# Kernel optimization log

Hardware: AMD Instinct MI355X
Metric: run time of the kernel (lower is better)

The kernel has to match this reference:

```python
import jax, jax.numpy as jnp
import numpy as np

MU = 0.99
THRESHOLD = 1.0


def setup_inputs() -> dict:
    key = jax.random.key(0)
    k1, k2, k3 = jax.random.split(key, 3)
    N, D, T, K = 8, 64, 8192, 2048
    x = jax.random.normal(k1, (N, D, T), dtype=jnp.float32)
    k = jax.random.normal(k2, (K, D), dtype=jnp.float32)
    k_sum = jax.random.normal(k3, (K, D), dtype=jnp.float32)
    k_elem = jnp.ones((K,), dtype=jnp.float32)
    return {"x": x, "k": k, "k_sum": k_sum, "k_elem": k_elem}


def reference(x, k, k_sum, k_elem):
    # x: [N, D, T] latents; k: [K, D] codebook; k_sum/k_elem: EMA buffers.
    N, D, T = x.shape
    K = k.shape[0]
    xf = x.transpose(0, 2, 1).reshape(-1, D)  # [NT, D]

    dist = (
        jnp.sum(xf * xf, axis=1, keepdims=True)
        - 2.0 * (xf @ k.T)
        + jnp.sum(k * k, axis=1)
    )
    codes = jnp.argmin(dist, axis=1)  # [NT] int
    xq = k[codes]                     # [NT, D] gather

    # Commitment loss + straight-through estimator
    commit = jnp.mean(jnp.square(jax.lax.stop_gradient(xq) - xf))
    xd = xf + jax.lax.stop_gradient(xq - xf)
    xd = xd.reshape(N, T, D).transpose(0, 2, 1)  # [N, D, T]

    # EMA codebook update (scatter) with usage threshold restart
    sum_new = jax.ops.segment_sum(xf, codes, num_segments=K)          # [K, D]
    cnt_new = jax.ops.segment_sum(jnp.ones((xf.shape[0],), xf.dtype), codes, num_segments=K)  # [K]
    k_sum_n = MU * k_sum + (1.0 - MU) * sum_new
    k_elem_n = MU * k_elem + (1.0 - MU) * cnt_new
    usage = (k_elem_n >= THRESHOLD).astype(xf.dtype)[:, None]
    k_new = usage * (k_sum_n / k_elem_n[:, None]) + (1.0 - usage) * k

    return xd, codes.reshape(N, T), commit, k_new, k_sum_n, k_elem_n
```

## Files before the change

kernel.cpp:

```cpp
#include <hip/hip_runtime.h>

#define DD 64
#define TT 8192
#define KK 2048
#define NTROWS 65536
#define TAUF 0.015f

#define OFF_CODES  4194304ull
#define OFF_COMMIT 4259840ull
#define OFF_KNEW   4259841ull
#define OFF_KSUM   4390913ull
#define OFF_KELEM  4521985ull

#define SQ(a) __fmul_rn((a), (a))

typedef short bf16x8 __attribute__((ext_vector_type(8)));
typedef float f32x4 __attribute__((ext_vector_type(4)));
typedef unsigned short ushort_t;

__device__ __forceinline__ ushort_t f2bf(float f) {
  unsigned u = __float_as_uint(f);
  unsigned r = u + 0x7fffu + ((u >> 16) & 1u);
  return (ushort_t)(r >> 16);
}
__device__ __forceinline__ float bf2f(ushort_t s) {
  return __uint_as_float(((unsigned)s) << 16);
}

__global__ __launch_bounds__(256) void vq_prep(const float* __restrict__ k,
                                               float* __restrict__ sk) {
  int c = blockIdx.x * 256 + threadIdx.x;
  if (c < KK) {
    const float* v = k + (size_t)c * DD;
    float r[8];
#pragma unroll
    for (int j = 0; j < 8; ++j) r[j] = SQ(v[j]);
#pragma unroll
    for (int i = 8; i < 64; i += 8) {
#pragma unroll
      for (int j = 0; j < 8; ++j) r[j] = __fadd_rn(r[j], SQ(v[i + j]));
    }
    sk[c] = __fadd_rn(
        __fadd_rn(__fadd_rn(r[0], r[1]), __fadd_rn(r[2], r[3])),
        __fadd_rn(__fadd_rn(r[4], r[5]), __fadd_rn(r[6], r[7])));
  }
}

__global__ __launch_bounds__(256) void vq_kprep(const float* __restrict__ k,
                                                ushort_t* __restrict__ kbh,
                                                ushort_t* __restrict__ kbl) {
  const int i = blockIdx.x * 256 + threadIdx.x;
  const float v = k[i];
  const ushort_t h = f2bf(v);
  kbh[i] = h;
  kbl[i] = f2bf(__fsub_rn(v, bf2f(h)));
}

__global__ __launch_bounds__(256)
__attribute__((amdgpu_waves_per_eu(2, 2)))
void vq_argmin_mfma(
    const float* __restrict__ x, const ushort_t* __restrict__ kbh,
    const ushort_t* __restrict__ kbl, const float* __restrict__ sk,
    float* __restrict__ out_codes, float* __restrict__ xf,
    int* __restrict__ susp_cnt, int* __restrict__ susp_rows) {
  __shared__ float xs[128][68];
  __shared__ ushort_t Bl[2][8192];
  __shared__ int slist[128];
  __shared__ int scnt, sbase;

  const int tid = threadIdx.x;
  const int lane = tid & 63;
  const int w = tid >> 6;
  const int g = lane >> 4;
  const int R0 = blockIdx.x * 128;
  const int n = R0 >> 13;
  const int t0 = R0 & (TT - 1);

  if (tid == 0) scnt = 0;

  {
    const float* xb = x + (size_t)n * (DD * TT) + t0;
    const int tt = tid & 127;
    const int dq = tid >> 7;
#pragma unroll
    for (int ch = 0; ch < 32; ++ch) {
      const int d = ch * 2 + dq;
      xs[tt][d] = xb[(size_t)d * TT + tt];
    }
  }

  const int c16 = tid & 15;
  const ushort_t* kbsel = (w >= 2) ? kbl : kbh;
  const int kch = w & 1;
  const ushort_t* bq0 = kbsel + ((size_t)(0 * 16 + c16) * 64 + kch * 32 + g * 8);
  const ushort_t* bq1 = kbsel + ((size_t)(1 * 16 + c16) * 64 + kch * 32 + g * 8);
  const ushort_t* bq2 = kbsel + ((size_t)(2 * 16 + c16) * 64 + kch * 32 + g * 8);
  const ushort_t* bq3 = kbsel + ((size_t)(3 * 16 + c16) * 64 + kch * 32 + g * 8);

  {
    int4 r0 = *(const int4*)bq0;
    int4 r1 = *(const int4*)bq1;
    int4 r2 = *(const int4*)bq2;
    int4 r3 = *(const int4*)bq3;
    *(int4*)&Bl[0][(0 * 256 + tid) * 8] = r0;
    *(int4*)&Bl[0][(1 * 256 + tid) * 8] = r1;
    *(int4*)&Bl[0][(2 * 256 + tid) * 8] = r2;
    *(int4*)&Bl[0][(3 * 256 + tid) * 8] = r3;
  }
  __syncthreads();

  {
    const int row = tid >> 1;
    const int half = tid & 1;
    float4* dst = (float4*)(xf + (size_t)(R0 + row) * DD + half * 32);
#pragma unroll
    for (int j = 0; j < 8; ++j) {
      dst[j] = make_float4(xs[row][half * 32 + 4 * j], xs[row][half * 32 + 4 * j + 1],
                           xs[row][half * 32 + 4 * j + 2], xs[row][half * 32 + 4 * j + 3]);
    }
  }

  union FR { bf16x8 v; ushort_t u[8]; };
  bf16x8 ahi00, ahi01, ahi10, ahi11, alo00, alo01, alo10, alo11;
#define CVT(J, VAL)                                   \
  { const float fv = (VAL); const ushort_t hb = f2bf(fv); \
    hh.u[J] = hb; ll.u[J] = f2bf(__fsub_rn(fv, bf2f(hb))); }
#define APREP(M, C, HN, LN)                            \
  { const int rowl = w * 32 + (M)*16 + (lane & 15);    \
    const int d0 = (C)*32 + g * 8;                     \
    const float4 v0 = *(const float4*)&xs[rowl][d0];   \
    const float4 v1 = *(const float4*)&xs[rowl][d0 + 4]; \
    FR hh, ll;                                         \
    CVT(0, v0.x) CVT(1, v0.y) CVT(2, v0.z) CVT(3, v0.w) \
    CVT(4, v1.x) CVT(5, v1.y) CVT(6, v1.z) CVT(7, v1.w) \
    HN = hh.v; LN = ll.v; }
  APREP(0, 0, ahi00, alo00)
  APREP(0, 1, ahi01, alo01)
  APREP(1, 0, ahi10, alo10)
  APREP(1, 1, ahi11, alo11)

  const float FMAXV = 3.402823466e38f;
  float m1_0 = FMAXV, m1_1 = FMAXV, m1_2 = FMAXV, m1_3 = FMAXV;
  float m1_4 = FMAXV, m1_5 = FMAXV, m1_6 = FMAXV, m1_7 = FMAXV;
  float m2_0 = FMAXV, m2_1 = FMAXV, m2_2 = FMAXV, m2_3 = FMAXV;
  float m2_4 = FMAXV, m2_5 = FMAXV, m2_6 = FMAXV, m2_7 = FMAXV;
  int i1_0 = 0, i1_1 = 0, i1_2 = 0, i1_3 = 0;
  int i1_4 = 0, i1_5 = 0, i1_6 = 0, i1_7 = 0;

#define TRACK(S, V)                                                   \
  { const float dd = fmaf(-2.0f, (V), skc);                           \
    const bool lt = dd < m1_##S;                                      \
    m2_##S = fminf(m2_##S, lt ? m1_##S : dd);                         \
    m1_##S = lt ? dd : m1_##S;                                        \
    i1_##S = lt ? codeIdx : i1_##S; }

#define MFMA(A, B, C) __builtin_amdgcn_mfma_f32_16x16x32_bf16((A), (B), (C), 0, 0, 0)

#define TILE(TT_)                                                              \
  {                                                                            \
    const int codeBase = p * 64 + (TT_)*16;                                    \
    const bf16x8 bh0 = *(const bf16x8*)&Bl[pb][((TT_)*256 + 0 * 64 + lane) * 8]; \
    const bf16x8 bh1 = *(const bf16x8*)&Bl[pb][((TT_)*256 + 1 * 64 + lane) * 8]; \
    const bf16x8 bl0 = *(const bf16x8*)&Bl[pb][((TT_)*256 + 2 * 64 + lane) * 8]; \
    const bf16x8 bl1 = *(const bf16x8*)&Bl[pb][((TT_)*256 + 3 * 64 + lane) * 8]; \
    f32x4 acc0 = {0.f, 0.f, 0.f, 0.f}, acc1 = {0.f, 0.f, 0.f, 0.f};            \
    acc0 = MFMA(ahi00, bh0, acc0); acc0 = MFMA(ahi01, bh1, acc0);              \
    acc0 = MFMA(ahi00, bl0, acc0); acc0 = MFMA(ahi01, bl1, acc0);              \
    acc0 = MFMA(alo00, bh0, acc0); acc0 = MFMA(alo01, bh1, acc0);              \
    acc1 = MFMA(ahi10, bh0, acc1); acc1 = MFMA(ahi11, bh1, acc1);              \
    acc1 = MFMA(ahi10, bl0, acc1); acc1 = MFMA(ahi11, bl1, acc1);              \
    acc1 = MFMA(alo10, bh0, acc1); acc1 = MFMA(alo11, bh1, acc1);              \
    const float skc = sk[codeBase + (lane & 15)];                              \
    const int codeIdx = codeBase + (lane & 15);                                \
    TRACK(0, acc0[0]) TRACK(1, acc0[1]) TRACK(2, acc0[2]) TRACK(3, acc0[3])    \
    TRACK(4, acc1[0]) TRACK(5, acc1[1]) TRACK(6, acc1[2]) TRACK(7, acc1[3])    \
  }

  int4 rg0, rg1, rg2, rg3;
  for (int p = 0; p < 32; ++p) {
    const int pb = p & 1;
    if (p < 31) {
      const size_t off = (size_t)(p + 1) * 4096;
      rg0 = *(const int4*)(bq0 + off);
      rg1 = *(const int4*)(bq1 + off);
      rg2 = *(const int4*)(bq2 + off);
      rg3 = *(const int4*)(bq3 + off);
    }
    TILE(0) TILE(1) TILE(2) TILE(3)
    __syncthreads();
    if (p < 31) {
      const int nb = pb ^ 1;
      *(int4*)&Bl[nb][(0 * 256 + tid) * 8] = rg0;
      *(int4*)&Bl[nb][(1 * 256 + tid) * 8] = rg1;
      *(int4*)&Bl[nb][(2 * 256 + tid) * 8] = rg2;
      *(int4*)&Bl[nb][(3 * 256 + tid) * 8] = rg3;
    }
    __syncthreads();
  }

#define REDSTEP(S, MASK)                                              \
  { const float o1 = __shfl_xor(m1_##S, MASK);                        \
    const int oi = __shfl_xor(i1_##S, MASK);                          \
    const float o2 = __shfl_xor(m2_##S, MASK);                        \
    const float hi2 = fmaxf(m1_##S, o1);                              \
    m2_##S = fminf(fminf(m2_##S, o2), hi2);                           \
    const bool tk = (o1 < m1_##S) || (o1 == m1_##S && oi < i1_##S);   \
    m1_##S = tk ? o1 : m1_##S;                                        \
    i1_##S = tk ? oi : i1_##S; }
#define RED(S) REDSTEP(S, 1) REDSTEP(S, 2) REDSTEP(S, 4) REDSTEP(S, 8)
  RED(0) RED(1) RED(2) RED(3) RED(4) RED(5) RED(6) RED(7)

  if ((lane & 15) == 0) {
#define WOUT(S, M, I)                                                   \
    { const int row = R0 + w * 32 + (M)*16 + g * 4 + (I);               \
      out_codes[row] = (float)i1_##S;                                   \
      if (m2_##S - m1_##S < TAUF) {                                     \
        const int pos = atomicAdd(&scnt, 1); slist[pos] = row; } }
    WOUT(0, 0, 0) WOUT(1, 0, 1) WOUT(2, 0, 2) WOUT(3, 0, 3)
    WOUT(4, 1, 0) WOUT(5, 1, 1) WOUT(6, 1, 2) WOUT(7, 1, 3)
  }
  __syncthreads();
  if (tid == 0 && scnt > 0) sbase = atomicAdd(susp_cnt, scnt);
  __syncthreads();
  for (int i = tid; i < scnt; i += 256) susp_rows[sbase + i] = slist[i];
}

__global__ __launch_bounds__(256) void vq_rescue(
    const float* __restrict__ xf, const float* __restrict__ k,
    const float* __restrict__ sk, const int* __restrict__ susp_cnt,
    const int* __restrict__ susp_rows, float* __restrict__ out_codes) {
  __shared__ float xs[4][64];
  const int lane = threadIdx.x & 63;
  const int wv = threadIdx.x >> 6;
  const int nsusp = *susp_cnt;
  const int nit = (nsusp + 8191) >> 13;

  for (int it = 0; it < nit; ++it) {
    const int si = it * 8192 + blockIdx.x * 4 + wv;
    const bool act = si < nsusp;
    int row = 0;
    if (act) {
      row = susp_rows[si];
      xs[wv][lane] = xf[(size_t)row * DD + lane];
    }
    __syncthreads();

    if (act) {
      float sumx;
      {
        float rr[8];
#pragma unroll
        for (int j = 0; j < 8; ++j) rr[j] = SQ(xs[wv][j]);
#pragma unroll
        for (int i = 8; i < 64; i += 8) {
#pragma unroll
          for (int j = 0; j < 8; ++j) rr[j] = __fadd_rn(rr[j], SQ(xs[wv][i + j]));
        }
        sumx = __fadd_rn(
            __fadd_rn(__fadd_rn(rr[0], rr[1]), __fadd_rn(rr[2], rr[3])),
            __fadd_rn(__fadd_rn(rr[4], rr[5]), __fadd_rn(rr[6], rr[7])));
      }

      float best = 3.402823466e38f;
      int bidx = lane;
#pragma unroll 4
      for (int i = 0; i < 32; ++i) {
        const int c = lane + i * 64;
        const float4* kp = (const float4*)(k + (size_t)c * DD);
        float a = 0.f;
#pragma unroll
        for (int j = 0; j < 16; ++j) {
          const float4 kv = kp[j];
          a = fmaf(xs[wv][4 * j + 0], kv.x, a);
          a = fmaf(xs[wv][4 * j + 1], kv.y, a);
          a = fmaf(xs[wv][4 * j + 2], kv.z, a);
          a = fmaf(xs[wv][4 * j + 3], kv.w, a);
        }
        const float dd = __fadd_rn(__fsub_rn(sumx, __fmul_rn(2.0f, a)), sk[c]);
        if (dd < best) { best = dd; bidx = c; }
      }

#pragma unroll
      for (int off = 1; off <= 32; off <<= 1) {
        const float ov = __shfl_xor(best, off);
        const int oi = __shfl_xor(bidx, off);
        if (ov < best || (ov == best && oi < bidx)) { best = ov; bidx = oi; }
      }
      if (lane == 0) out_codes[row] = (float)bidx;
    }
    __syncthreads();
  }
}

__global__ __launch_bounds__(256) void vq_count(const float* __restrict__ codes_f,
                                                int* __restrict__ cnt_int) {
  const int row = blockIdx.x * 256 + threadIdx.x;
  atomicAdd(&cnt_int[(int)codes_f[row]], 1);
}

__global__ __launch_bounds__(256) void vq_scan(const int* __restrict__ cnt_int,
                                               int* __restrict__ cursor) {
  __shared__ int sm[256];
  const int t = threadIdx.x;
  int v[8];
  int tot = 0;
#pragma unroll
  for (int j = 0; j < 8; ++j) { v[j] = cnt_int[t * 8 + j]; tot += v[j]; }
  sm[t] = tot;
  __syncthreads();
  int val = tot;
  for (int off = 1; off < 256; off <<= 1) {
    const int add = (t >= off) ? sm[t - off] : 0;
    __syncthreads();
    val += add;
    sm[t] = val;
    __syncthreads();
  }
  int base = val - tot;
#pragma unroll
  for (int j = 0; j < 8; ++j) { cursor[t * 8 + j] = base; base += v[j]; }
}

__global__ __launch_bounds__(256) void vq_scatteridx(
    const float* __restrict__ codes_f, int* __restrict__ cursor,
    unsigned* __restrict__ bucket) {
  const int row = blockIdx.x * 256 + threadIdx.x;
  const int code = (int)codes_f[row];
  const int pos = atomicAdd(&cursor[code], 1);
  bucket[pos] = ((unsigned)code << 16) | (unsigned)row;
}

__global__ __launch_bounds__(256) void vq_codesum(
    const float* __restrict__ xf, const unsigned* __restrict__ bucket,
    float* __restrict__ out_ksum) {
  __shared__ unsigned sh[4][64];
  const int lane = threadIdx.x & 63;
  const int wv = threadIdx.x >> 6;
  const int base = (blockIdx.x * 4 + wv) * 64;

  sh[wv][lane] = bucket[base + lane];
  __syncthreads();

  float acc = 0.f;
  int cur = (int)(sh[wv][0] >> 16);
#pragma unroll
  for (int b = 0; b < 8; ++b) {
    float xv[8];
    int cd[8];
#pragma unroll
    for (int j = 0; j < 8; ++j) {
      const unsigned p = sh[wv][b * 8 + j];
      cd[j] = (int)(p >> 16);
      xv[j] = xf[(size_t)(p & 0xFFFFu) * DD + lane];
    }
#pragma unroll
    for (int j = 0; j < 8; ++j) {
      if (cd[j] != cur) {
        atomicAdd(&out_ksum[(size_t)cur * DD + lane], acc);
        acc = 0.f;
        cur = cd[j];
      }
      acc = __fadd_rn(acc, xv[j]);
    }
  }
  atomicAdd(&out_ksum[(size_t)cur * DD + lane], acc);
}

__global__ __launch_bounds__(256) void vq_epi(
    const float* __restrict__ x, const float* __restrict__ k,
    const float* __restrict__ codes_f, float* __restrict__ out_xd,
    float* __restrict__ partial) {
  const int lane = threadIdx.x & 63;
  const int q = threadIdx.x >> 6;
  const int row = blockIdx.x * 64 + lane;
  const int n = row >> 13;
  const int t = row & (TT - 1);
  const int d0 = blockIdx.y * 16 + q * 4;

  const int code = (int)codes_f[row];

  const float* xp = x + (size_t)n * (DD * TT) + t;
  float* xd_base = out_xd + (size_t)n * (DD * TT) + t;

  const float4 kq = ((const float4*)k)[(size_t)code * 16 + (d0 >> 2)];

  float csum = 0.f;
#pragma unroll
  for (int j = 0; j < 4; ++j) {
    const int d = d0 + j;
    const float xqv = (j == 0) ? kq.x : (j == 1) ? kq.y : (j == 2) ? kq.z : kq.w;
    const float xv = xp[(size_t)d * TT];
    const float diff = __fsub_rn(xqv, xv);
    xd_base[(size_t)d * TT] = __fadd_rn(xv, diff);
    csum = fmaf(diff, diff, csum);
  }

  __shared__ float cs[4];
#pragma unroll
  for (int off = 32; off >= 1; off >>= 1) csum += __shfl_xor(csum, off);
  if (lane == 0) cs[q] = csum;
  __syncthreads();
  if (threadIdx.x == 0) {
    partial[blockIdx.y * 1024 + blockIdx.x] = (cs[0] + cs[1]) + (cs[2] + cs[3]);
  }
}

__global__ __launch_bounds__(256) void vq_finalize(
    const float* __restrict__ k, const float* __restrict__ k_sum,
    const float* __restrict__ k_elem, const int* __restrict__ cnt_int,
    const float* __restrict__ partial, float* __restrict__ out_commit,
    float* __restrict__ out_knew, float* __restrict__ out_ksum,
    float* __restrict__ out_kelem) {
  const int i = blockIdx.x * 256 + threadIdx.x;

  if (blockIdx.x == 0) {
    __shared__ float red[256];
    float s = 0.f;
#pragma unroll
    for (int j = 0; j < 16; ++j) s += partial[threadIdx.x * 16 + j];
    red[threadIdx.x] = s;
    __syncthreads();
    for (int off = 128; off >= 1; off >>= 1) {
      if (threadIdx.x < off) red[threadIdx.x] += red[threadIdx.x + off];
      __syncthreads();
    }
    if (threadIdx.x == 0) out_commit[0] = red[0] / 4194304.0f;
  }

  if (i < KK * DD) {
    const int c = i >> 6;
    const float cnt = (float)cnt_int[c];
    const float ke_n = __fadd_rn(__fmul_rn(0.99f, k_elem[c]), __fmul_rn(0.01f, cnt));
    const float s_raw = out_ksum[i];
    const float ks_n = __fadd_rn(__fmul_rn(0.99f, k_sum[i]), __fmul_rn(0.01f, s_raw));
    out_ksum[i] = ks_n;
    out_knew[i] = (ke_n >= 1.0f) ? (ks_n / ke_n) : k[i];
    if ((i & 63) == 0) out_kelem[c] = ke_n;
  }
}

extern "C" void kernel_launch(void* const* d_in, const int* in_sizes, int n_in,
                              void* d_out, int out_size, void* d_ws, size_t ws_size,
                              hipStream_t stream) {
  const float* x = (const float*)d_in[0];
  const float* k = (const float*)d_in[1];
  const float* k_sum = (const float*)d_in[2];
  const float* k_elem = (const float*)d_in[3];

  float* out = (float*)d_out;
  float* out_xd = out;
  float* out_codes = out + OFF_CODES;
  float* out_commit = out + OFF_COMMIT;
  float* out_knew = out + OFF_KNEW;
  float* out_ksum = out + OFF_KSUM;
  float* out_kelem = out + OFF_KELEM;

  ushort_t* kbh = (ushort_t*)(((size_t)(out + OFF_KNEW) + 15) & ~(size_t)15);
  ushort_t* kbl = kbh + (size_t)KK * DD;

  char* ws = (char*)d_ws;
  float* sk = (float*)ws;
  int* cnt_int = (int*)(ws + 8192);
  int* cursor = (int*)(ws + 16384);
  float* partial = (float*)(ws + 24576);
  unsigned* bucket = (unsigned*)(ws + 40960);
  int* susp_cnt = cursor;
  int* susp_rows = (int*)bucket;

  hipMemsetAsync(cnt_int, 0, (size_t)KK * sizeof(int), stream);
  hipMemsetAsync(susp_cnt, 0, sizeof(int), stream);

  vq_prep<<<(KK + 255) / 256, 256, 0, stream>>>(k, sk);
  vq_kprep<<<(KK * DD) / 256, 256, 0, stream>>>(k, kbh, kbl);

  vq_argmin_mfma<<<NTROWS / 128, 256, 0, stream>>>(x, kbh, kbl, sk, out_codes,
                                                   out_xd, susp_cnt, susp_rows);

  hipMemsetAsync(out_ksum, 0, (size_t)KK * DD * sizeof(float), stream);

  vq_rescue<<<2048, 256, 0, stream>>>(out_xd, k, sk, susp_cnt, susp_rows,
                                      out_codes);

  vq_count<<<NTROWS / 256, 256, 0, stream>>>(out_codes, cnt_int);
  vq_scan<<<1, 256, 0, stream>>>(cnt_int, cursor);
  vq_scatteridx<<<NTROWS / 256, 256, 0, stream>>>(out_codes, cursor, bucket);
  vq_codesum<<<NTROWS / 256, 256, 0, stream>>>(out_xd, bucket, out_ksum);

  dim3 epi_grid(NTROWS / 64, 4);
  vq_epi<<<epi_grid, 256, 0, stream>>>(x, k, out_codes, out_xd, partial);

  vq_finalize<<<(KK * DD + 255) / 256, 256, 0, stream>>>(
      k, k_sum, k_elem, cnt_int, partial, out_commit, out_knew, out_ksum,
      out_kelem);
}
```

Before: 204.3 us.

## Halve argmin tile rows, alias LDS, raise occupancy, fuse code counting

The MFMA argmin kernel now processes 64 rows per block instead of 128. The x staging buffer and the codebook double buffer share one aliased 32KB LDS region, which cuts per-block LDS and registers so waves_per_eu can rise from 2 to 4. One barrier per codebook panel is removed. Code histogram counting moves into the argmin and rescue kernels, dropping the separate vq_count launch. The trade-off is that each block reloads the whole codebook for half as many rows, which doubles codebook L2 traffic.

```diff
diff --git a/kernel.cpp b/kernel.cpp
--- a/kernel.cpp
+++ b/kernel.cpp
@@ -57,37 +57,28 @@
 }
 
 __global__ __launch_bounds__(256)
-__attribute__((amdgpu_waves_per_eu(2, 2)))
+__attribute__((amdgpu_waves_per_eu(4, 4)))
 void vq_argmin_mfma(
     const float* __restrict__ x, const ushort_t* __restrict__ kbh,
     const ushort_t* __restrict__ kbl, const float* __restrict__ sk,
     float* __restrict__ out_codes, float* __restrict__ xf,
-    int* __restrict__ susp_cnt, int* __restrict__ susp_rows) {
-  __shared__ float xs[128][68];
-  __shared__ ushort_t Bl[2][8192];
-  __shared__ int slist[128];
+    int* __restrict__ susp_cnt, int* __restrict__ susp_rows,
+    int* __restrict__ cnt_int) {
+  __shared__ __align__(16) char smraw[32768];
+  float (*xs)[68] = (float(*)[68])smraw;
+  ushort_t (*Bl)[8192] = (ushort_t(*)[8192])smraw;
+  __shared__ int slist[64];
   __shared__ int scnt, sbase;
 
   const int tid = threadIdx.x;
   const int lane = tid & 63;
   const int w = tid >> 6;
   const int g = lane >> 4;
-  const int R0 = blockIdx.x * 128;
+  const int R0 = blockIdx.x * 64;
   const int n = R0 >> 13;
   const int t0 = R0 & (TT - 1);
 
   if (tid == 0) scnt = 0;
-
-  {
-    const float* xb = x + (size_t)n * (DD * TT) + t0;
-    const int tt = tid & 127;
-    const int dq = tid >> 7;
-#pragma unroll
-    for (int ch = 0; ch < 32; ++ch) {
-      const int d = ch * 2 + dq;
-      xs[tt][d] = xb[(size_t)d * TT + tt];
-    }
-  }
 
   const int c16 = tid & 15;
   const ushort_t* kbsel = (w >= 2) ? kbl : kbh;
@@ -96,37 +87,41 @@
   const ushort_t* bq1 = kbsel + ((size_t)(1 * 16 + c16) * 64 + kch * 32 + g * 8);
   const ushort_t* bq2 = kbsel + ((size_t)(2 * 16 + c16) * 64 + kch * 32 + g * 8);
   const ushort_t* bq3 = kbsel + ((size_t)(3 * 16 + c16) * 64 + kch * 32 + g * 8);
+  int4 rg0 = *(const int4*)bq0;
+  int4 rg1 = *(const int4*)bq1;
+  int4 rg2 = *(const int4*)bq2;
+  int4 rg3 = *(const int4*)bq3;
 
   {
-    int4 r0 = *(const int4*)bq0;
-    int4 r1 = *(const int4*)bq1;
-    int4 r2 = *(const int4*)bq2;
-    int4 r3 = *(const int4*)bq3;
-    *(int4*)&Bl[0][(0 * 256 + tid) * 8] = r0;
-    *(int4*)&Bl[0][(1 * 256 + tid) * 8] = r1;
-    *(int4*)&Bl[0][(2 * 256 + tid) * 8] = r2;
-    *(int4*)&Bl[0][(3 * 256 + tid) * 8] = r3;
+    const float* xb = x + (size_t)n * (DD * TT) + t0;
+    const int tt = tid & 63;
+    const int dq = tid >> 6;
+#pragma unroll
+    for (int ch = 0; ch < 16; ++ch) {
+      const int d = ch * 4 + dq;
+      xs[tt][d] = xb[(size_t)d * TT + tt];
+    }
   }
   __syncthreads();
 
   {
-    const int row = tid >> 1;
-    const int half = tid & 1;
-    float4* dst = (float4*)(xf + (size_t)(R0 + row) * DD + half * 32);
-#pragma unroll
-    for (int j = 0; j < 8; ++j) {
-      dst[j] = make_float4(xs[row][half * 32 + 4 * j], xs[row][half * 32 + 4 * j + 1],
-                           xs[row][half * 32 + 4 * j + 2], xs[row][half * 32 + 4 * j + 3]);
+    const int row = tid >> 2;
+    const int dq = (tid & 3) * 16;
+    float4* dst = (float4*)(xf + (size_t)(R0 + row) * DD + dq);
+#pragma unroll
+    for (int j = 0; j < 4; ++j) {
+      dst[j] = make_float4(xs[row][dq + 4 * j], xs[row][dq + 4 * j + 1],
+                           xs[row][dq + 4 * j + 2], xs[row][dq + 4 * j + 3]);
     }
   }
 
   union FR { bf16x8 v; ushort_t u[8]; };
-  bf16x8 ahi00, ahi01, ahi10, ahi11, alo00, alo01, alo10, alo11;
+  bf16x8 ahi0, ahi1, alo0, alo1;
 #define CVT(J, VAL)                                   \
   { const float fv = (VAL); const ushort_t hb = f2bf(fv); \
     hh.u[J] = hb; ll.u[J] = f2bf(__fsub_rn(fv, bf2f(hb))); }
-#define APREP(M, C, HN, LN)                            \
-  { const int rowl = w * 32 + (M)*16 + (lane & 15);    \
+#define APREP(C, HN, LN)                               \
+  { const int rowl = w * 16 + (lane & 15);             \
     const int d0 = (C)*32 + g * 8;                     \
     const float4 v0 = *(const float4*)&xs[rowl][d0];   \
     const float4 v1 = *(const float4*)&xs[rowl][d0 + 4]; \
@@ -134,18 +129,21 @@
     CVT(0, v0.x) CVT(1, v0.y) CVT(2, v0.z) CVT(3, v0.w) \
     CVT(4, v1.x) CVT(5, v1.y) CVT(6, v1.z) CVT(7, v1.w) \
     HN = hh.v; LN = ll.v; }
-  APREP(0, 0, ahi00, alo00)
-  APREP(0, 1, ahi01, alo01)
-  APREP(1, 0, ahi10, alo10)
-  APREP(1, 1, ahi11, alo11)
+  APREP(0, ahi0, alo0)
+  APREP(1, ahi1, alo1)
+
+  __syncthreads();
+
+  *(int4*)&Bl[0][(0 * 256 + tid) * 8] = rg0;
+  *(int4*)&Bl[0][(1 * 256 + tid) * 8] = rg1;
+  *(int4*)&Bl[0][(2 * 256 + tid) * 8] = rg2;
+  *(int4*)&Bl[0][(3 * 256 + tid) * 8] = rg3;
+  __syncthreads();
 
   const float FMAXV = 3.402823466e38f;
   float m1_0 = FMAXV, m1_1 = FMAXV, m1_2 = FMAXV, m1_3 = FMAXV;
-  float m1_4 = FMAXV, m1_5 = FMAXV, m1_6 = FMAXV, m1_7 = FMAXV;
   float m2_0 = FMAXV, m2_1 = FMAXV, m2_2 = FMAXV, m2_3 = FMAXV;
-  float m2_4 = FMAXV, m2_5 = FMAXV, m2_6 = FMAXV, m2_7 = FMAXV;
   int i1_0 = 0, i1_1 = 0, i1_2 = 0, i1_3 = 0;
-  int i1_4 = 0, i1_5 = 0, i1_6 = 0, i1_7 = 0;
 
 #define TRACK(S, V)                                                   \
   { const float dd = fmaf(-2.0f, (V), skc);                           \
@@ -163,20 +161,15 @@
     const bf16x8 bh1 = *(const bf16x8*)&Bl[pb][((TT_)*256 + 1 * 64 + lane) * 8]; \
     const bf16x8 bl0 = *(const bf16x8*)&Bl[pb][((TT_)*256 + 2 * 64 + lane) * 8]; \
     const bf16x8 bl1 = *(const bf16x8*)&Bl[pb][((TT_)*256 + 3 * 64 + lane) * 8]; \
-    f32x4 acc0 = {0.f, 0.f, 0.f, 0.f}, acc1 = {0.f, 0.f, 0.f, 0.f};            \
-    acc0 = MFMA(ahi00, bh0, acc0); acc0 = MFMA(ahi01, bh1, acc0);              \
-    acc0 = MFMA(ahi00, bl0, acc0); acc0 = MFMA(ahi01, bl1, acc0);              \
-    acc0 = MFMA(alo00, bh0, acc0); acc0 = MFMA(alo01, bh1, acc0);              \
-    acc1 = MFMA(ahi10, bh0, acc1); acc1 = MFMA(ahi11, bh1, acc1);              \
-    acc1 = MFMA(ahi10, bl0, acc1); acc1 = MFMA(ahi11, bl1, acc1);              \
-    acc1 = MFMA(alo10, bh0, acc1); acc1 = MFMA(alo11, bh1, acc1);              \
+    f32x4 acc = {0.f, 0.f, 0.f, 0.f};                                          \
+    acc = MFMA(ahi0, bh0, acc); acc = MFMA(ahi1, bh1, acc);                    \
+    acc = MFMA(ahi0, bl0, acc); acc = MFMA(ahi1, bl1, acc);                    \
+    acc = MFMA(alo0, bh0, acc); acc = MFMA(alo1, bh1, acc);                    \
     const float skc = sk[codeBase + (lane & 15)];                              \
     const int codeIdx = codeBase + (lane & 15);                                \
-    TRACK(0, acc0[0]) TRACK(1, acc0[1]) TRACK(2, acc0[2]) TRACK(3, acc0[3])    \
-    TRACK(4, acc1[0]) TRACK(5, acc1[1]) TRACK(6, acc1[2]) TRACK(7, acc1[3])    \
-  }
-
-  int4 rg0, rg1, rg2, rg3;
+    TRACK(0, acc[0]) TRACK(1, acc[1]) TRACK(2, acc[2]) TRACK(3, acc[3])        \
+  }
+
   for (int p = 0; p < 32; ++p) {
     const int pb = p & 1;
     if (p < 31) {
@@ -187,7 +180,6 @@
       rg3 = *(const int4*)(bq3 + off);
     }
     TILE(0) TILE(1) TILE(2) TILE(3)
-    __syncthreads();
     if (p < 31) {
       const int nb = pb ^ 1;
       *(int4*)&Bl[nb][(0 * 256 + tid) * 8] = rg0;
@@ -208,16 +200,18 @@
     m1_##S = tk ? o1 : m1_##S;                                        \
     i1_##S = tk ? oi : i1_##S; }
 #define RED(S) REDSTEP(S, 1) REDSTEP(S, 2) REDSTEP(S, 4) REDSTEP(S, 8)
-  RED(0) RED(1) RED(2) RED(3) RED(4) RED(5) RED(6) RED(7)
+  RED(0) RED(1) RED(2) RED(3)
 
   if ((lane & 15) == 0) {
-#define WOUT(S, M, I)                                                   \
-    { const int row = R0 + w * 32 + (M)*16 + g * 4 + (I);               \
+#define WOUT(S, I)                                                      \
+    { const int row = R0 + w * 16 + g * 4 + (I);                        \
       out_codes[row] = (float)i1_##S;                                   \
       if (m2_##S - m1_##S < TAUF) {                                     \
-        const int pos = atomicAdd(&scnt, 1); slist[pos] = row; } }
-    WOUT(0, 0, 0) WOUT(1, 0, 1) WOUT(2, 0, 2) WOUT(3, 0, 3)
-    WOUT(4, 1, 0) WOUT(5, 1, 1) WOUT(6, 1, 2) WOUT(7, 1, 3)
+        const int pos = atomicAdd(&scnt, 1); slist[pos] = row;          \
+      } else {                                                          \
+        atomicAdd(&cnt_int[i1_##S], 1);                                 \
+      } }
+    WOUT(0, 0) WOUT(1, 1) WOUT(2, 2) WOUT(3, 3)
   }
   __syncthreads();
   if (tid == 0 && scnt > 0) sbase = atomicAdd(susp_cnt, scnt);
@@ -228,7 +222,8 @@
 __global__ __launch_bounds__(256) void vq_rescue(
     const float* __restrict__ xf, const float* __restrict__ k,
     const float* __restrict__ sk, const int* __restrict__ susp_cnt,
-    const int* __restrict__ susp_rows, float* __restrict__ out_codes) {
+    const int* __restrict__ susp_rows, float* __restrict__ out_codes,
+    int* __restrict__ cnt_int) {
   __shared__ float xs[4][64];
   const int lane = threadIdx.x & 63;
   const int wv = threadIdx.x >> 6;
@@ -286,16 +281,13 @@
         const int oi = __shfl_xor(bidx, off);
         if (ov < best || (ov == best && oi < bidx)) { best = ov; bidx = oi; }
       }
-      if (lane == 0) out_codes[row] = (float)bidx;
-    }
-    __syncthreads();
-  }
-}
-
-__global__ __launch_bounds__(256) void vq_count(const float* __restrict__ codes_f,
-                                                int* __restrict__ cnt_int) {
-  const int row = blockIdx.x * 256 + threadIdx.x;
-  atomicAdd(&cnt_int[(int)codes_f[row]], 1);
+      if (lane == 0) {
+        out_codes[row] = (float)bidx;
+        atomicAdd(&cnt_int[bidx], 1);
+      }
+    }
+    __syncthreads();
+  }
 }
 
 __global__ __launch_bounds__(256) void vq_scan(const int* __restrict__ cnt_int,
@@ -473,15 +465,15 @@
   vq_prep<<<(KK + 255) / 256, 256, 0, stream>>>(k, sk);
   vq_kprep<<<(KK * DD) / 256, 256, 0, stream>>>(k, kbh, kbl);
 
-  vq_argmin_mfma<<<NTROWS / 128, 256, 0, stream>>>(x, kbh, kbl, sk, out_codes,
-                                                   out_xd, susp_cnt, susp_rows);
+  vq_argmin_mfma<<<NTROWS / 64, 256, 0, stream>>>(x, kbh, kbl, sk, out_codes,
+                                                  out_xd, susp_cnt, susp_rows,
+                                                  cnt_int);
 
   hipMemsetAsync(out_ksum, 0, (size_t)KK * DD * sizeof(float), stream);
 
   vq_rescue<<<2048, 256, 0, stream>>>(out_xd, k, sk, susp_cnt, susp_rows,
-                                      out_codes);
-
-  vq_count<<<NTROWS / 256, 256, 0, stream>>>(out_codes, cnt_int);
+                                      out_codes, cnt_int);
+
   vq_scan<<<1, 256, 0, stream>>>(cnt_int, cursor);
   vq_scatteridx<<<NTROWS / 256, 256, 0, stream>>>(out_codes, cursor, bucket);
   vq_codesum<<<NTROWS / 256, 256, 0, stream>>>(out_xd, bucket, out_ksum);
```

Result: no change. 206.7 us (+1.2%).

## Load codebook fragments directly from global and fuse code counting into argmin

Applied to the files above, without the earlier changes.

The argmin kernel no longer stages the bf16 hi/lo codebook through double-buffered shared memory with two barriers per step. Each lane now loads its MFMA B fragments straight from global memory, relying on L1/L2 caching of the small codebook. The separate count kernel is removed: confident rows are counted with atomics in the argmin kernel and rescued rows in the rescue kernel. This removes barriers, LDS traffic and one launch, but exposes global-load latency in the MFMA loop and adds contended atomics.

```diff
diff --git a/kernel.cpp b/kernel.cpp
--- a/kernel.cpp
+++ b/kernel.cpp
@@ -62,9 +62,9 @@
     const float* __restrict__ x, const ushort_t* __restrict__ kbh,
     const ushort_t* __restrict__ kbl, const float* __restrict__ sk,
     float* __restrict__ out_codes, float* __restrict__ xf,
-    int* __restrict__ susp_cnt, int* __restrict__ susp_rows) {
+    int* __restrict__ susp_cnt, int* __restrict__ susp_rows,
+    int* __restrict__ cnt_int) {
   __shared__ float xs[128][68];
-  __shared__ ushort_t Bl[2][8192];
   __shared__ int slist[128];
   __shared__ int scnt, sbase;
 
@@ -72,6 +72,7 @@
   const int lane = tid & 63;
   const int w = tid >> 6;
   const int g = lane >> 4;
+  const int c16 = lane & 15;
   const int R0 = blockIdx.x * 128;
   const int n = R0 >> 13;
   const int t0 = R0 & (TT - 1);
@@ -87,25 +88,6 @@
       const int d = ch * 2 + dq;
       xs[tt][d] = xb[(size_t)d * TT + tt];
     }
-  }
-
-  const int c16 = tid & 15;
-  const ushort_t* kbsel = (w >= 2) ? kbl : kbh;
-  const int kch = w & 1;
-  const ushort_t* bq0 = kbsel + ((size_t)(0 * 16 + c16) * 64 + kch * 32 + g * 8);
-  const ushort_t* bq1 = kbsel + ((size_t)(1 * 16 + c16) * 64 + kch * 32 + g * 8);
-  const ushort_t* bq2 = kbsel + ((size_t)(2 * 16 + c16) * 64 + kch * 32 + g * 8);
-  const ushort_t* bq3 = kbsel + ((size_t)(3 * 16 + c16) * 64 + kch * 32 + g * 8);
-
-  {
-    int4 r0 = *(const int4*)bq0;
-    int4 r1 = *(const int4*)bq1;
-    int4 r2 = *(const int4*)bq2;
-    int4 r3 = *(const int4*)bq3;
-    *(int4*)&Bl[0][(0 * 256 + tid) * 8] = r0;
-    *(int4*)&Bl[0][(1 * 256 + tid) * 8] = r1;
-    *(int4*)&Bl[0][(2 * 256 + tid) * 8] = r2;
-    *(int4*)&Bl[0][(3 * 256 + tid) * 8] = r3;
   }
   __syncthreads();
 
@@ -126,7 +108,7 @@
   { const float fv = (VAL); const ushort_t hb = f2bf(fv); \
     hh.u[J] = hb; ll.u[J] = f2bf(__fsub_rn(fv, bf2f(hb))); }
 #define APREP(M, C, HN, LN)                            \
-  { const int rowl = w * 32 + (M)*16 + (lane & 15);    \
+  { const int rowl = w * 32 + (M)*16 + c16;            \
     const int d0 = (C)*32 + g * 8;                     \
     const float4 v0 = *(const float4*)&xs[rowl][d0];   \
     const float4 v1 = *(const float4*)&xs[rowl][d0 + 4]; \
@@ -139,6 +121,9 @@
   APREP(1, 0, ahi10, alo10)
   APREP(1, 1, ahi11, alo11)
 
+  const ushort_t* phh = kbh + (size_t)c16 * 64 + g * 8;
+  const ushort_t* pll = kbl + (size_t)c16 * 64 + g * 8;
+
   const float FMAXV = 3.402823466e38f;
   float m1_0 = FMAXV, m1_1 = FMAXV, m1_2 = FMAXV, m1_3 = FMAXV;
   float m1_4 = FMAXV, m1_5 = FMAXV, m1_6 = FMAXV, m1_7 = FMAXV;
@@ -159,10 +144,11 @@
 #define TILE(TT_)                                                              \
   {                                                                            \
     const int codeBase = p * 64 + (TT_)*16;                                    \
-    const bf16x8 bh0 = *(const bf16x8*)&Bl[pb][((TT_)*256 + 0 * 64 + lane) * 8]; \
-    const bf16x8 bh1 = *(const bf16x8*)&Bl[pb][((TT_)*256 + 1 * 64 + lane) * 8]; \
-    const bf16x8 bl0 = *(const bf16x8*)&Bl[pb][((TT_)*256 + 2 * 64 + lane) * 8]; \
-    const bf16x8 bl1 = *(const bf16x8*)&Bl[pb][((TT_)*256 + 3 * 64 + lane) * 8]; \
+    const size_t eoff = (size_t)codeBase * 64;                                 \
+    const bf16x8 bh0 = *(const bf16x8*)(phh + eoff);                           \
+    const bf16x8 bh1 = *(const bf16x8*)(phh + eoff + 32);                      \
+    const bf16x8 bl0 = *(const bf16x8*)(pll + eoff);                           \
+    const bf16x8 bl1 = *(const bf16x8*)(pll + eoff + 32);                      \
     f32x4 acc0 = {0.f, 0.f, 0.f, 0.f}, acc1 = {0.f, 0.f, 0.f, 0.f};            \
     acc0 = MFMA(ahi00, bh0, acc0); acc0 = MFMA(ahi01, bh1, acc0);              \
     acc0 = MFMA(ahi00, bl0, acc0); acc0 = MFMA(ahi01, bl1, acc0);              \
@@ -170,32 +156,14 @@
     acc1 = MFMA(ahi10, bh0, acc1); acc1 = MFMA(ahi11, bh1, acc1);              \
     acc1 = MFMA(ahi10, bl0, acc1); acc1 = MFMA(ahi11, bl1, acc1);              \
     acc1 = MFMA(alo10, bh0, acc1); acc1 = MFMA(alo11, bh1, acc1);              \
-    const float skc = sk[codeBase + (lane & 15)];                              \
-    const int codeIdx = codeBase + (lane & 15);                                \
+    const float skc = sk[codeBase + c16];                                      \
+    const int codeIdx = codeBase + c16;                                        \
     TRACK(0, acc0[0]) TRACK(1, acc0[1]) TRACK(2, acc0[2]) TRACK(3, acc0[3])    \
     TRACK(4, acc1[0]) TRACK(5, acc1[1]) TRACK(6, acc1[2]) TRACK(7, acc1[3])    \
   }
 
-  int4 rg0, rg1, rg2, rg3;
   for (int p = 0; p < 32; ++p) {
-    const int pb = p & 1;
-    if (p < 31) {
-      const size_t off = (size_t)(p + 1) * 4096;
-      rg0 = *(const int4*)(bq0 + off);
-      rg1 = *(const int4*)(bq1 + off);
-      rg2 = *(const int4*)(bq2 + off);
-      rg3 = *(const int4*)(bq3 + off);
-    }
     TILE(0) TILE(1) TILE(2) TILE(3)
-    __syncthreads();
-    if (p < 31) {
-      const int nb = pb ^ 1;
-      *(int4*)&Bl[nb][(0 * 256 + tid) * 8] = rg0;
-      *(int4*)&Bl[nb][(1 * 256 + tid) * 8] = rg1;
-      *(int4*)&Bl[nb][(2 * 256 + tid) * 8] = rg2;
-      *(int4*)&Bl[nb][(3 * 256 + tid) * 8] = rg3;
-    }
-    __syncthreads();
   }
 
 #define REDSTEP(S, MASK)                                              \
@@ -210,12 +178,15 @@
 #define RED(S) REDSTEP(S, 1) REDSTEP(S, 2) REDSTEP(S, 4) REDSTEP(S, 8)
   RED(0) RED(1) RED(2) RED(3) RED(4) RED(5) RED(6) RED(7)
 
-  if ((lane & 15) == 0) {
+  if (c16 == 0) {
 #define WOUT(S, M, I)                                                   \
     { const int row = R0 + w * 32 + (M)*16 + g * 4 + (I);               \
       out_codes[row] = (float)i1_##S;                                   \
       if (m2_##S - m1_##S < TAUF) {                                     \
-        const int pos = atomicAdd(&scnt, 1); slist[pos] = row; } }
+        const int pos = atomicAdd(&scnt, 1); slist[pos] = row;          \
+      } else {                                                          \
+        atomicAdd(&cnt_int[i1_##S], 1);                                 \
+      } }
     WOUT(0, 0, 0) WOUT(1, 0, 1) WOUT(2, 0, 2) WOUT(3, 0, 3)
     WOUT(4, 1, 0) WOUT(5, 1, 1) WOUT(6, 1, 2) WOUT(7, 1, 3)
   }
@@ -228,7 +199,8 @@
 __global__ __launch_bounds__(256) void vq_rescue(
     const float* __restrict__ xf, const float* __restrict__ k,
     const float* __restrict__ sk, const int* __restrict__ susp_cnt,
-    const int* __restrict__ susp_rows, float* __restrict__ out_codes) {
+    const int* __restrict__ susp_rows, float* __restrict__ out_codes,
+    int* __restrict__ cnt_int) {
   __shared__ float xs[4][64];
   const int lane = threadIdx.x & 63;
   const int wv = threadIdx.x >> 6;
@@ -286,16 +258,13 @@
         const int oi = __shfl_xor(bidx, off);
         if (ov < best || (ov == best && oi < bidx)) { best = ov; bidx = oi; }
       }
-      if (lane == 0) out_codes[row] = (float)bidx;
+      if (lane == 0) {
+        out_codes[row] = (float)bidx;
+        atomicAdd(&cnt_int[bidx], 1);
+      }
     }
     __syncthreads();
   }
-}
-
-__global__ __launch_bounds__(256) void vq_count(const float* __restrict__ codes_f,
-                                                int* __restrict__ cnt_int) {
-  const int row = blockIdx.x * 256 + threadIdx.x;
-  atomicAdd(&cnt_int[(int)codes_f[row]], 1);
 }
 
 __global__ __launch_bounds__(256) void vq_scan(const int* __restrict__ cnt_int,
@@ -474,14 +443,14 @@
   vq_kprep<<<(KK * DD) / 256, 256, 0, stream>>>(k, kbh, kbl);
 
   vq_argmin_mfma<<<NTROWS / 128, 256, 0, stream>>>(x, kbh, kbl, sk, out_codes,
-                                                   out_xd, susp_cnt, susp_rows);
+                                                   out_xd, susp_cnt, susp_rows,
+                                                   cnt_int);
 
   hipMemsetAsync(out_ksum, 0, (size_t)KK * DD * sizeof(float), stream);
 
   vq_rescue<<<2048, 256, 0, stream>>>(out_xd, k, sk, susp_cnt, susp_rows,
-                                      out_codes);
-
-  vq_count<<<NTROWS / 256, 256, 0, stream>>>(out_codes, cnt_int);
+                                      out_codes, cnt_int);
+
   vq_scan<<<1, 256, 0, stream>>>(cnt_int, cursor);
   vq_scatteridx<<<NTROWS / 256, 256, 0, stream>>>(out_codes, cursor, bucket);
   vq_codesum<<<NTROWS / 256, 256, 0, stream>>>(out_xd, bucket, out_ksum);
```

Measured after the change: 272.0 us. +33.1%, slower.

## Use two waves per block with 64 rows each to raise B-fragment reuse

Applied to the files above, without the earlier changes.

The argmin kernel drops from four waves to two per 128-row block. Each wave now covers 64 rows instead of 32 and reuses every codebook B fragment read from LDS across four MFMA row tiles. Each wave also handles both K halves for its hi or lo codebook split. This halves LDS B reads per MFMA and interleaves independent accumulators to hide MFMA latency, at the cost of more VGPRs, one wave per EU, and fewer threads for the global loads and stores.

```diff
diff --git a/kernel.cpp b/kernel.cpp
--- a/kernel.cpp
+++ b/kernel.cpp
@@ -56,8 +56,8 @@
   kbl[i] = f2bf(__fsub_rn(v, bf2f(h)));
 }
 
-__global__ __launch_bounds__(256)
-__attribute__((amdgpu_waves_per_eu(2, 2)))
+__global__ __launch_bounds__(128)
+__attribute__((amdgpu_waves_per_eu(1, 1)))
 void vq_argmin_mfma(
     const float* __restrict__ x, const ushort_t* __restrict__ kbh,
     const ushort_t* __restrict__ kbl, const float* __restrict__ sk,
@@ -72,6 +72,7 @@
   const int lane = tid & 63;
   const int w = tid >> 6;
   const int g = lane >> 4;
+  const int c16 = lane & 15;
   const int R0 = blockIdx.x * 128;
   const int n = R0 >> 13;
   const int t0 = R0 & (TT - 1);
@@ -80,53 +81,53 @@
 
   {
     const float* xb = x + (size_t)n * (DD * TT) + t0;
-    const int tt = tid & 127;
-    const int dq = tid >> 7;
-#pragma unroll
-    for (int ch = 0; ch < 32; ++ch) {
-      const int d = ch * 2 + dq;
-      xs[tt][d] = xb[(size_t)d * TT + tt];
-    }
-  }
-
-  const int c16 = tid & 15;
-  const ushort_t* kbsel = (w >= 2) ? kbl : kbh;
-  const int kch = w & 1;
-  const ushort_t* bq0 = kbsel + ((size_t)(0 * 16 + c16) * 64 + kch * 32 + g * 8);
-  const ushort_t* bq1 = kbsel + ((size_t)(1 * 16 + c16) * 64 + kch * 32 + g * 8);
-  const ushort_t* bq2 = kbsel + ((size_t)(2 * 16 + c16) * 64 + kch * 32 + g * 8);
-  const ushort_t* bq3 = kbsel + ((size_t)(3 * 16 + c16) * 64 + kch * 32 + g * 8);
+#pragma unroll
+    for (int d = 0; d < 64; ++d) xs[tid][d] = xb[(size_t)d * TT + tid];
+  }
+
+  const ushort_t* kbsel = w ? kbl : kbh;
+  const ushort_t* bqA0 = kbsel + ((size_t)(0 * 16 + c16) * 64 + 0 * 32 + g * 8);
+  const ushort_t* bqA1 = kbsel + ((size_t)(0 * 16 + c16) * 64 + 1 * 32 + g * 8);
+  const ushort_t* bqB0 = kbsel + ((size_t)(1 * 16 + c16) * 64 + 0 * 32 + g * 8);
+  const ushort_t* bqB1 = kbsel + ((size_t)(1 * 16 + c16) * 64 + 1 * 32 + g * 8);
+  const ushort_t* bqC0 = kbsel + ((size_t)(2 * 16 + c16) * 64 + 0 * 32 + g * 8);
+  const ushort_t* bqC1 = kbsel + ((size_t)(2 * 16 + c16) * 64 + 1 * 32 + g * 8);
+  const ushort_t* bqD0 = kbsel + ((size_t)(3 * 16 + c16) * 64 + 0 * 32 + g * 8);
+  const ushort_t* bqD1 = kbsel + ((size_t)(3 * 16 + c16) * 64 + 1 * 32 + g * 8);
 
   {
-    int4 r0 = *(const int4*)bq0;
-    int4 r1 = *(const int4*)bq1;
-    int4 r2 = *(const int4*)bq2;
-    int4 r3 = *(const int4*)bq3;
-    *(int4*)&Bl[0][(0 * 256 + tid) * 8] = r0;
-    *(int4*)&Bl[0][(1 * 256 + tid) * 8] = r1;
-    *(int4*)&Bl[0][(2 * 256 + tid) * 8] = r2;
-    *(int4*)&Bl[0][(3 * 256 + tid) * 8] = r3;
+    int4 rA0 = *(const int4*)bqA0, rA1 = *(const int4*)bqA1;
+    int4 rB0 = *(const int4*)bqB0, rB1 = *(const int4*)bqB1;
+    int4 rC0 = *(const int4*)bqC0, rC1 = *(const int4*)bqC1;
+    int4 rD0 = *(const int4*)bqD0, rD1 = *(const int4*)bqD1;
+    *(int4*)&Bl[0][(0 * 256 + (2 * w + 0) * 64 + lane) * 8] = rA0;
+    *(int4*)&Bl[0][(0 * 256 + (2 * w + 1) * 64 + lane) * 8] = rA1;
+    *(int4*)&Bl[0][(1 * 256 + (2 * w + 0) * 64 + lane) * 8] = rB0;
+    *(int4*)&Bl[0][(1 * 256 + (2 * w + 1) * 64 + lane) * 8] = rB1;
+    *(int4*)&Bl[0][(2 * 256 + (2 * w + 0) * 64 + lane) * 8] = rC0;
+    *(int4*)&Bl[0][(2 * 256 + (2 * w + 1) * 64 + lane) * 8] = rC1;
+    *(int4*)&Bl[0][(3 * 256 + (2 * w + 0) * 64 + lane) * 8] = rD0;
+    *(int4*)&Bl[0][(3 * 256 + (2 * w + 1) * 64 + lane) * 8] = rD1;
   }
   __syncthreads();
 
   {
-    const int row = tid >> 1;
-    const int half = tid & 1;
-    float4* dst = (float4*)(xf + (size_t)(R0 + row) * DD + half * 32);
-#pragma unroll
-    for (int j = 0; j < 8; ++j) {
-      dst[j] = make_float4(xs[row][half * 32 + 4 * j], xs[row][half * 32 + 4 * j + 1],
-                           xs[row][half * 32 + 4 * j + 2], xs[row][half * 32 + 4 * j + 3]);
+    float4* dst = (float4*)(xf + (size_t)(R0 + tid) * DD);
+#pragma unroll
+    for (int j = 0; j < 16; ++j) {
+      dst[j] = make_float4(xs[tid][4 * j], xs[tid][4 * j + 1],
+                           xs[tid][4 * j + 2], xs[tid][4 * j + 3]);
     }
   }
 
   union FR { bf16x8 v; ushort_t u[8]; };
-  bf16x8 ahi00, ahi01, ahi10, ahi11, alo00, alo01, alo10, alo11;
+  bf16x8 AH00, AH01, AH10, AH11, AH20, AH21, AH30, AH31;
+  bf16x8 AL00, AL01, AL10, AL11, AL20, AL21, AL30, AL31;
 #define CVT(J, VAL)                                   \
   { const float fv = (VAL); const ushort_t hb = f2bf(fv); \
     hh.u[J] = hb; ll.u[J] = f2bf(__fsub_rn(fv, bf2f(hb))); }
 #define APREP(M, C, HN, LN)                            \
-  { const int rowl = w * 32 + (M)*16 + (lane & 15);    \
+  { const int rowl = w * 64 + (M)*16 + c16;            \
     const int d0 = (C)*32 + g * 8;                     \
     const float4 v0 = *(const float4*)&xs[rowl][d0];   \
     const float4 v1 = *(const float4*)&xs[rowl][d0 + 4]; \
@@ -134,18 +135,24 @@
     CVT(0, v0.x) CVT(1, v0.y) CVT(2, v0.z) CVT(3, v0.w) \
     CVT(4, v1.x) CVT(5, v1.y) CVT(6, v1.z) CVT(7, v1.w) \
     HN = hh.v; LN = ll.v; }
-  APREP(0, 0, ahi00, alo00)
-  APREP(0, 1, ahi01, alo01)
-  APREP(1, 0, ahi10, alo10)
-  APREP(1, 1, ahi11, alo11)
+  APREP(0, 0, AH00, AL00) APREP(0, 1, AH01, AL01)
+  APREP(1, 0, AH10, AL10) APREP(1, 1, AH11, AL11)
+  APREP(2, 0, AH20, AL20) APREP(2, 1, AH21, AL21)
+  APREP(3, 0, AH30, AL30) APREP(3, 1, AH31, AL31)
 
   const float FMAXV = 3.402823466e38f;
   float m1_0 = FMAXV, m1_1 = FMAXV, m1_2 = FMAXV, m1_3 = FMAXV;
   float m1_4 = FMAXV, m1_5 = FMAXV, m1_6 = FMAXV, m1_7 = FMAXV;
+  float m1_8 = FMAXV, m1_9 = FMAXV, m1_10 = FMAXV, m1_11 = FMAXV;
+  float m1_12 = FMAXV, m1_13 = FMAXV, m1_14 = FMAXV, m1_15 = FMAXV;
   float m2_0 = FMAXV, m2_1 = FMAXV, m2_2 = FMAXV, m2_3 = FMAXV;
   float m2_4 = FMAXV, m2_5 = FMAXV, m2_6 = FMAXV, m2_7 = FMAXV;
+  float m2_8 = FMAXV, m2_9 = FMAXV, m2_10 = FMAXV, m2_11 = FMAXV;
+  float m2_12 = FMAXV, m2_13 = FMAXV, m2_14 = FMAXV, m2_15 = FMAXV;
   int i1_0 = 0, i1_1 = 0, i1_2 = 0, i1_3 = 0;
   int i1_4 = 0, i1_5 = 0, i1_6 = 0, i1_7 = 0;
+  int i1_8 = 0, i1_9 = 0, i1_10 = 0, i1_11 = 0;
+  int i1_12 = 0, i1_13 = 0, i1_14 = 0, i1_15 = 0;
 
 #define TRACK(S, V)                                                   \
   { const float dd = fmaf(-2.0f, (V), skc);                           \
@@ -163,37 +170,50 @@
     const bf16x8 bh1 = *(const bf16x8*)&Bl[pb][((TT_)*256 + 1 * 64 + lane) * 8]; \
     const bf16x8 bl0 = *(const bf16x8*)&Bl[pb][((TT_)*256 + 2 * 64 + lane) * 8]; \
     const bf16x8 bl1 = *(const bf16x8*)&Bl[pb][((TT_)*256 + 3 * 64 + lane) * 8]; \
-    f32x4 acc0 = {0.f, 0.f, 0.f, 0.f}, acc1 = {0.f, 0.f, 0.f, 0.f};            \
-    acc0 = MFMA(ahi00, bh0, acc0); acc0 = MFMA(ahi01, bh1, acc0);              \
-    acc0 = MFMA(ahi00, bl0, acc0); acc0 = MFMA(ahi01, bl1, acc0);              \
-    acc0 = MFMA(alo00, bh0, acc0); acc0 = MFMA(alo01, bh1, acc0);              \
-    acc1 = MFMA(ahi10, bh0, acc1); acc1 = MFMA(ahi11, bh1, acc1);              \
-    acc1 = MFMA(ahi10, bl0, acc1); acc1 = MFMA(ahi11, bl1, acc1);              \
-    acc1 = MFMA(alo10, bh0, acc1); acc1 = MFMA(alo11, bh1, acc1);              \
-    const float skc = sk[codeBase + (lane & 15)];                              \
-    const int codeIdx = codeBase + (lane & 15);                                \
-    TRACK(0, acc0[0]) TRACK(1, acc0[1]) TRACK(2, acc0[2]) TRACK(3, acc0[3])    \
-    TRACK(4, acc1[0]) TRACK(5, acc1[1]) TRACK(6, acc1[2]) TRACK(7, acc1[3])    \
-  }
-
-  int4 rg0, rg1, rg2, rg3;
+    f32x4 a0 = {0.f, 0.f, 0.f, 0.f}, a1 = {0.f, 0.f, 0.f, 0.f};                \
+    f32x4 a2 = {0.f, 0.f, 0.f, 0.f}, a3 = {0.f, 0.f, 0.f, 0.f};                \
+    a0 = MFMA(AH00, bh0, a0); a1 = MFMA(AH10, bh0, a1);                        \
+    a2 = MFMA(AH20, bh0, a2); a3 = MFMA(AH30, bh0, a3);                        \
+    a0 = MFMA(AH01, bh1, a0); a1 = MFMA(AH11, bh1, a1);                        \
+    a2 = MFMA(AH21, bh1, a2); a3 = MFMA(AH31, bh1, a3);                        \
+    a0 = MFMA(AH00, bl0, a0); a1 = MFMA(AH10, bl0, a1);                        \
+    a2 = MFMA(AH20, bl0, a2); a3 = MFMA(AH30, bl0, a3);                        \
+    a0 = MFMA(AH01, bl1, a0); a1 = MFMA(AH11, bl1, a1);                        \
+    a2 = MFMA(AH21, bl1, a2); a3 = MFMA(AH31, bl1, a3);                        \
+    a0 = MFMA(AL00, bh0, a0); a1 = MFMA(AL10, bh0, a1);                        \
+    a2 = MFMA(AL20, bh0, a2); a3 = MFMA(AL30, bh0, a3);                        \
+    a0 = MFMA(AL01, bh1, a0); a1 = MFMA(AL11, bh1, a1);                        \
+    a2 = MFMA(AL21, bh1, a2); a3 = MFMA(AL31, bh1, a3);                        \
+    const float skc = sk[codeBase + c16];                                      \
+    const int codeIdx = codeBase + c16;                                        \
+    TRACK(0, a0[0]) TRACK(1, a0[1]) TRACK(2, a0[2]) TRACK(3, a0[3])            \
+    TRACK(4, a1[0]) TRACK(5, a1[1]) TRACK(6, a1[2]) TRACK(7, a1[3])            \
+    TRACK(8, a2[0]) TRACK(9, a2[1]) TRACK(10, a2[2]) TRACK(11, a2[3])          \
+    TRACK(12, a3[0]) TRACK(13, a3[1]) TRACK(14, a3[2]) TRACK(15, a3[3])        \
+  }
+
+  int4 rA0, rA1, rB0, rB1, rC0, rC1, rD0, rD1;
   for (int p = 0; p < 32; ++p) {
     const int pb = p & 1;
     if (p < 31) {
       const size_t off = (size_t)(p + 1) * 4096;
-      rg0 = *(const int4*)(bq0 + off);
-      rg1 = *(const int4*)(bq1 + off);
-      rg2 = *(const int4*)(bq2 + off);
-      rg3 = *(const int4*)(bq3 + off);
+      rA0 = *(const int4*)(bqA0 + off); rA1 = *(const int4*)(bqA1 + off);
+      rB0 = *(const int4*)(bqB0 + off); rB1 = *(const int4*)(bqB1 + off);
+      rC0 = *(const int4*)(bqC0 + off); rC1 = *(const int4*)(bqC1 + off);
+      rD0 = *(const int4*)(bqD0 + off); rD1 = *(const int4*)(bqD1 + off);
     }
     TILE(0) TILE(1) TILE(2) TILE(3)
     __syncthreads();
     if (p < 31) {
       const int nb = pb ^ 1;
-      *(int4*)&Bl[nb][(0 * 256 + tid) * 8] = rg0;
-      *(int4*)&Bl[nb][(1 * 256 + tid) * 8] = rg1;
-      *(int4*)&Bl[nb][(2 * 256 + tid) * 8] = rg2;
-      *(int4*)&Bl[nb][(3 * 256 + tid) * 8] = rg3;
+      *(int4*)&Bl[nb][(0 * 256 + (2 * w + 0) * 64 + lane) * 8] = rA0;
+      *(int4*)&Bl[nb][(0 * 256 + (2 * w + 1) * 64 + lane) * 8] = rA1;
+      *(int4*)&Bl[nb][(1 * 256 + (2 * w + 0) * 64 + lane) * 8] = rB0;
+      *(int4*)&Bl[nb][(1 * 256 + (2 * w + 1) * 64 + lane) * 8] = rB1;
+      *(int4*)&Bl[nb][(2 * 256 + (2 * w + 0) * 64 + lane) * 8] = rC0;
+      *(int4*)&Bl[nb][(2 * 256 + (2 * w + 1) * 64 + lane) * 8] = rC1;
+      *(int4*)&Bl[nb][(3 * 256 + (2 * w + 0) * 64 + lane) * 8] = rD0;
+      *(int4*)&Bl[nb][(3 * 256 + (2 * w + 1) * 64 + lane) * 8] = rD1;
     }
     __syncthreads();
   }
@@ -209,20 +229,23 @@
     i1_##S = tk ? oi : i1_##S; }
 #define RED(S) REDSTEP(S, 1) REDSTEP(S, 2) REDSTEP(S, 4) REDSTEP(S, 8)
   RED(0) RED(1) RED(2) RED(3) RED(4) RED(5) RED(6) RED(7)
-
-  if ((lane & 15) == 0) {
+  RED(8) RED(9) RED(10) RED(11) RED(12) RED(13) RED(14) RED(15)
+
+  if (c16 == 0) {
 #define WOUT(S, M, I)                                                   \
-    { const int row = R0 + w * 32 + (M)*16 + g * 4 + (I);               \
+    { const int row = R0 + w * 64 + (M)*16 + g * 4 + (I);               \
       out_codes[row] = (float)i1_##S;                                   \
       if (m2_##S - m1_##S < TAUF) {                                     \
         const int pos = atomicAdd(&scnt, 1); slist[pos] = row; } }
     WOUT(0, 0, 0) WOUT(1, 0, 1) WOUT(2, 0, 2) WOUT(3, 0, 3)
     WOUT(4, 1, 0) WOUT(5, 1, 1) WOUT(6, 1, 2) WOUT(7, 1, 3)
+    WOUT(8, 2, 0) WOUT(9, 2, 1) WOUT(10, 2, 2) WOUT(11, 2, 3)
+    WOUT(12, 3, 0) WOUT(13, 3, 1) WOUT(14, 3, 2) WOUT(15, 3, 3)
   }
   __syncthreads();
   if (tid == 0 && scnt > 0) sbase = atomicAdd(susp_cnt, scnt);
   __syncthreads();
-  for (int i = tid; i < scnt; i += 256) susp_rows[sbase + i] = slist[i];
+  for (int i = tid; i < scnt; i += 128) susp_rows[sbase + i] = slist[i];
 }
 
 __global__ __launch_bounds__(256) void vq_rescue(
@@ -473,7 +496,7 @@
   vq_prep<<<(KK + 255) / 256, 256, 0, stream>>>(k, sk);
   vq_kprep<<<(KK * DD) / 256, 256, 0, stream>>>(k, kbh, kbl);
 
-  vq_argmin_mfma<<<NTROWS / 128, 256, 0, stream>>>(x, kbh, kbl, sk, out_codes,
+  vq_argmin_mfma<<<NTROWS / 128, 128, 0, stream>>>(x, kbh, kbl, sk, out_codes,
                                                    out_xd, susp_cnt, susp_rows);
 
   hipMemsetAsync(out_ksum, 0, (size_t)KK * DD * sizeof(float), stream);
```

After: 242.6 us. +18.7%, slower.
